# Kernel tuning notes

Hardware: AMD Instinct MI355X
Metric: run time of the kernel (lower is better)

## Reference

```python
import jax, jax.numpy as jnp
import numpy as np

EPS = 1e-5
NUM_GROUPS = 32
NUM_HEADS = 8

def group_norm(x, w, b):
    # x: (B, C, H, W), 32 groups, affine per-channel
    B, C, H, W = x.shape
    xg = x.reshape(B, NUM_GROUPS, C // NUM_GROUPS, H, W)
    mu = xg.mean(axis=(2, 3, 4), keepdims=True)
    var = xg.var(axis=(2, 3, 4), keepdims=True)
    xn = ((xg - mu) * jax.lax.rsqrt(var + EPS)).reshape(B, C, H, W)
    return xn * w[None, :, None, None] + b[None, :, None, None]

def conv1x1(x, w, b):
    # 1x1 conv == per-pixel linear; w: (out, in), x: (B, C, H, W)
    return jnp.einsum('oc,bchw->bohw', w, x) + b[None, :, None, None]

def setup_inputs() -> dict:
    key = jax.random.key(0)
    ks = jax.random.split(key, 4)
    B, C, H, W = 2, 512, 64, 64
    s = 1.0 / np.sqrt(C)
    return {
        'x': jax.random.normal(ks[0], (B, C, H, W), jnp.float32),
        'gn_w': jnp.ones((C,), jnp.float32),
        'gn_b': jnp.zeros((C,), jnp.float32),
        'wq': jax.random.normal(ks[1], (C, C), jnp.float32) * s,
        'bq': jnp.zeros((C,), jnp.float32),
        'wkv': jax.random.normal(ks[2], (2 * C, C), jnp.float32) * s,
        'bkv': jnp.zeros((2 * C,), jnp.float32),
        'wo': jax.random.normal(ks[3], (C, C), jnp.float32) * s,
        'bo': jnp.zeros((C,), jnp.float32),
    }

def reference(x, gn_w, gn_b, wq, bq, wkv, bkv, wo, bo):
    B, C, H, W = x.shape
    hd = C // NUM_HEADS  # head_dim
    residual = x
    x_norm = group_norm(x, gn_w, gn_b)
    q = conv1x1(x_norm, wq, bq).reshape(B, NUM_HEADS, hd, H * W)
    kv = conv1x1(x_norm, wkv, bkv)
    k, v = jnp.split(kv, 2, axis=1)
    k = k.reshape(B, NUM_HEADS, hd, H * W)
    v = v.reshape(B, NUM_HEADS, hd, H * W)
    scale = hd ** (-0.5)
    attn = jnp.einsum('bhdi,bhdj->bhij', q, k) * scale
    attn = jax.nn.softmax(attn, axis=-1)
    out = jnp.einsum('bhij,bhdj->bhdi', attn, v).reshape(B, C, H, W)
    out = conv1x1(out, wo, bo)
    return out + residual
```

## Files before the change

### kernel.cpp

```cpp
#include <hip/hip_runtime.h>
#include <cmath>

typedef __bf16 bf16x8 __attribute__((ext_vector_type(8)));
typedef __bf16 bf16x4 __attribute__((ext_vector_type(4)));
typedef float  f32x4  __attribute__((ext_vector_type(4)));

static __device__ __forceinline__ f32x4 mfma16(bf16x8 a, bf16x8 b, f32x4 c) {
    return __builtin_amdgcn_mfma_f32_16x16x32_bf16(a, b, c, 0, 0, 0);
}

static __device__ __forceinline__ float fast_exp2(float x) {
#if __has_builtin(__builtin_amdgcn_exp2f)
    return __builtin_amdgcn_exp2f(x);
#else
    return exp2f(x);
#endif
}

#define OFF_STATS 0
#define OFF_W     4096
#define OFF_XNT   (OFF_W + 2u*1024*1024)
#define OFF_QKT   (OFF_XNT + 8u*1024*1024)
#define OFF_V     (OFF_QKT + 16u*1024*1024)
#define OFF_OP    (OFF_V + 8u*1024*1024)
#define CHUNK_O   4194304u
#define CHUNK_L   65536u

__global__ __launch_bounds__(256) void cvt_w(const float* __restrict__ wq,
                                             const float* __restrict__ wkv,
                                             const float* __restrict__ wo,
                                             __bf16* __restrict__ dst) {
    int i = blockIdx.x * 256 + threadIdx.x;
    if (i < 262144)      dst[i] = (__bf16)wq[i];
    else if (i < 786432) dst[i] = (__bf16)wkv[i - 262144];
    else                 dst[i] = (__bf16)wo[i - 786432];
}

__global__ __launch_bounds__(256) void gn_stats(const float* __restrict__ x,
                                                float* __restrict__ stats) {
    int blk = blockIdx.x;
    int bg = blk >> 2, chunk = blk & 3;
    const float* base = x + (size_t)bg * 65536 + (size_t)chunk * 16384;
    float s = 0.f, ss = 0.f;
    for (int i = threadIdx.x; i < 4096; i += 256) {
        float4 v = ((const float4*)base)[i];
        s  += v.x + v.y + v.z + v.w;
        ss += v.x*v.x + v.y*v.y + v.z*v.z + v.w*v.w;
    }
    #pragma unroll
    for (int off = 1; off < 64; off <<= 1) {
        s  += __shfl_xor(s,  off);
        ss += __shfl_xor(ss, off);
    }
    __shared__ float red[8];
    int wave = threadIdx.x >> 6;
    if ((threadIdx.x & 63) == 0) { red[wave*2] = s; red[wave*2+1] = ss; }
    __syncthreads();
    if (threadIdx.x == 0) {
        float S  = red[0] + red[2] + red[4] + red[6];
        float SS = red[1] + red[3] + red[5] + red[7];
        atomicAdd(&stats[bg*2],     S);
        atomicAdd(&stats[bg*2 + 1], SS);
    }
}

__global__ __launch_bounds__(256) void gn_apply(const float* __restrict__ x,
                                                const float* __restrict__ stats,
                                                const float* __restrict__ w,
                                                const float* __restrict__ bgn,
                                                __bf16* __restrict__ xnT) {
    int p0 = blockIdx.x * 64, c0 = blockIdx.y * 64, b = blockIdx.z;
    int tid = threadIdx.x, lane = tid & 63, wave = tid >> 6;
    __shared__ float t[64][69];
    #pragma unroll
    for (int i = 0; i < 16; ++i) {
        int cc = i * 4 + wave;
        int c  = c0 + cc;
        int g  = (b << 5) + (c >> 4);
        float mu  = stats[g*2] * (1.f/65536.f);
        float var = stats[g*2+1] * (1.f/65536.f) - mu*mu;
        float rstd = rsqrtf(var + 1e-5f);
        float val = x[((size_t)(b*512 + c) << 12) + p0 + lane];
        t[cc][lane] = (val - mu) * rstd * w[c] + bgn[c];
    }
    __syncthreads();
    #pragma unroll
    for (int i = 0; i < 16; ++i) {
        int pp = i * 4 + wave;
        xnT[((size_t)(b*4096 + p0 + pp) << 9) + c0 + lane] = (__bf16)t[lane][pp];
    }
}

__global__ __launch_bounds__(256) void gemm128_kernel(
    const __bf16* __restrict__ A, const __bf16* __restrict__ B,
    const float* __restrict__ bias, const float* __restrict__ bias2, int nsplit,
    float scale0, void* __restrict__ out,
    int N, int K, long long strideA, long long strideO) {
    const int bz = blockIdx.z;
    A += strideA * bz;
    const int m0 = blockIdx.x * 128, n0 = blockIdx.y * 128;
    const int tid = threadIdx.x, lane = tid & 63, wave = tid >> 6;
    const int quad = lane >> 4, l16 = lane & 15;
    const int wm = (wave >> 1) * 64, wn = (wave & 1) * 64;

    __shared__ __attribute__((aligned(16))) __bf16 lds_a[128][40];
    __shared__ __attribute__((aligned(16))) __bf16 lds_b[128][40];

    f32x4 acc[4][4];
    #pragma unroll
    for (int mt = 0; mt < 4; ++mt)
        #pragma unroll
        for (int nt = 0; nt < 4; ++nt)
            #pragma unroll
            for (int r = 0; r < 4; ++r) acc[mt][nt][r] = 0.f;

    const int row_s = tid >> 2;
    const int kc    = (tid & 3) << 3;

    uint4 ra0, ra1, rb0, rb1;
    const __bf16* Abase = A + (size_t)(m0 + row_s) * K + kc;
    const __bf16* Bbase = B + (size_t)(n0 + row_s) * K + kc;
    ra0 = *(const uint4*)Abase;
    ra1 = *(const uint4*)(Abase + (size_t)64 * K);
    rb0 = *(const uint4*)Bbase;
    rb1 = *(const uint4*)(Bbase + (size_t)64 * K);

    for (int kt = 0; kt < K; kt += 32) {
        *(uint4*)&lds_a[row_s][kc]      = ra0;
        *(uint4*)&lds_a[row_s + 64][kc] = ra1;
        *(uint4*)&lds_b[row_s][kc]      = rb0;
        *(uint4*)&lds_b[row_s + 64][kc] = rb1;
        __syncthreads();
        if (kt + 32 < K) {
            ra0 = *(const uint4*)(Abase + kt + 32);
            ra1 = *(const uint4*)(Abase + kt + 32 + (size_t)64 * K);
            rb0 = *(const uint4*)(Bbase + kt + 32);
            rb1 = *(const uint4*)(Bbase + kt + 32 + (size_t)64 * K);
        }
        bf16x8 af[4], bfr[4];
        #pragma unroll
        for (int mt = 0; mt < 4; ++mt)
            af[mt] = *(const bf16x8*)&lds_a[wm + mt*16 + l16][quad*8];
        #pragma unroll
        for (int nt = 0; nt < 4; ++nt)
            bfr[nt] = *(const bf16x8*)&lds_b[wn + nt*16 + l16][quad*8];
        #pragma unroll
        for (int mt = 0; mt < 4; ++mt)
            #pragma unroll
            for (int nt = 0; nt < 4; ++nt)
                acc[mt][nt] = mfma16(af[mt], bfr[nt], acc[mt][nt]);
        __syncthreads();
    }

    #pragma unroll
    for (int mt = 0; mt < 4; ++mt) {
        const int mrow = m0 + wm + mt*16 + quad*4;
        #pragma unroll
        for (int nt = 0; nt < 4; ++nt) {
            const int ncol = n0 + wn + nt*16 + l16;
            #pragma unroll
            for (int r = 0; r < 4; ++r) {
                const int m = mrow + r;
                float bval = (ncol < nsplit) ? bias[ncol] : bias2[ncol - nsplit];
                float val = acc[mt][nt][r] + bval;
                if (ncol < nsplit) val *= scale0;
                ((__bf16*)out)[(size_t)strideO * bz + (size_t)m * N + ncol] = (__bf16)val;
            }
        }
    }
}

template<int OUT_F32, int HAS_RES>
__global__ __launch_bounds__(256) void gemm64_kernel(
    const __bf16* __restrict__ A, const __bf16* __restrict__ B,
    const float* __restrict__ bias, const float* __restrict__ res,
    void* __restrict__ out,
    int N, int K, long long strideB, long long strideO) {
    const int bz = blockIdx.z;
    B += strideB * bz;
    const int m0 = blockIdx.x * 64, n0 = blockIdx.y * 128;
    const int tid = threadIdx.x, lane = tid & 63, wave = tid >> 6;
    const int quad = lane >> 4, l16 = lane & 15;
    const int wn = wave * 32;

    __shared__ __attribute__((aligned(16))) __bf16 lds_a[64][40];
    __shared__ __attribute__((aligned(16))) __bf16 lds_b[128][40];

    f32x4 acc[4][2];
    #pragma unroll
    for (int mt = 0; mt < 4; ++mt)
        #pragma unroll
        for (int nt = 0; nt < 2; ++nt)
            #pragma unroll
            for (int r = 0; r < 4; ++r) acc[mt][nt][r] = 0.f;

    const int row_s = tid >> 2;
    const int kc    = (tid & 3) << 3;

    uint4 ra0, rb0, rb1;
    const __bf16* Abase = A + (size_t)(m0 + row_s) * K + kc;
    const __bf16* Bbase = B + (size_t)(n0 + row_s) * K + kc;
    ra0 = *(const uint4*)Abase;
    rb0 = *(const uint4*)Bbase;
    rb1 = *(const uint4*)(Bbase + (size_t)64 * K);

    for (int kt = 0; kt < K; kt += 32) {
        *(uint4*)&lds_a[row_s][kc]      = ra0;
        *(uint4*)&lds_b[row_s][kc]      = rb0;
        *(uint4*)&lds_b[row_s + 64][kc] = rb1;
        __syncthreads();
        if (kt + 32 < K) {
            ra0 = *(const uint4*)(Abase + kt + 32);
            rb0 = *(const uint4*)(Bbase + kt + 32);
            rb1 = *(const uint4*)(Bbase + kt + 32 + (size_t)64 * K);
        }
        bf16x8 af[4], bfr[2];
        #pragma unroll
        for (int mt = 0; mt < 4; ++mt)
            af[mt] = *(const bf16x8*)&lds_a[mt*16 + l16][quad*8];
        #pragma unroll
        for (int nt = 0; nt < 2; ++nt)
            bfr[nt] = *(const bf16x8*)&lds_b[wn + nt*16 + l16][quad*8];
        #pragma unroll
        for (int mt = 0; mt < 4; ++mt)
            #pragma unroll
            for (int nt = 0; nt < 2; ++nt)
                acc[mt][nt] = mfma16(af[mt], bfr[nt], acc[mt][nt]);
        __syncthreads();
    }

    #pragma unroll
    for (int mt = 0; mt < 4; ++mt) {
        const int mrow = m0 + mt*16 + quad*4;
        #pragma unroll
        for (int nt = 0; nt < 2; ++nt) {
            const int ncol = n0 + wn + nt*16 + l16;
            #pragma unroll
            for (int r = 0; r < 4; ++r) {
                const int m = mrow + r;
                float val = acc[mt][nt][r] + bias[m];
                const size_t idx = (size_t)strideO * bz + (size_t)m * N + ncol;
                if constexpr (HAS_RES) val += res[idx];
                if constexpr (OUT_F32) ((float*)out)[idx] = val;
                else ((__bf16*)out)[idx] = (__bf16)val;
            }
        }
    }
}

template<int NCH>
__global__ __launch_bounds__(256, 3) void attn_kernel(const __bf16* __restrict__ qkT,
                                                      const __bf16* __restrict__ v,
                                                      __bf16* __restrict__ attnT,
                                                      __bf16* __restrict__ Opart,
                                                      float* __restrict__ Lpart) {
    const int b = blockIdx.y >> 3, h = blockIdx.y & 7;
    const int chunk = (NCH > 1) ? blockIdx.z : 0;
    const int NITER = 64 / NCH;
    const int kt0 = chunk * (4096 / NCH);
    const int tid = threadIdx.x;
    const int wave = tid >> 6, lane = tid & 63;
    const int quad = lane >> 4, l16 = lane & 15;
    const int qbase = blockIdx.x * 256 + wave * 64;

    const __bf16* qkTb = qkT + ((size_t)b << 22);
    const __bf16* vb   = v   + ((size_t)b << 21);

    __shared__ __attribute__((aligned(16))) __bf16 lds_k[64][64];
    __shared__ __attribute__((aligned(16))) __bf16 lds_v[80][64];
    __shared__ __attribute__((aligned(16))) __bf16 lds_p[4][64][68];

    bf16x8 aq[4][2];
    #pragma unroll
    for (int mt = 0; mt < 4; ++mt) {
        const __bf16* qrow = qkTb + (size_t)(qbase + mt*16 + l16) * 1024 + h*64 + quad*8;
        aq[mt][0] = *(const bf16x8*)qrow;
        aq[mt][1] = *(const bf16x8*)(qrow + 32);
    }
    f32x4 o[4][5];
    #pragma unroll
    for (int mt = 0; mt < 4; ++mt)
        #pragma unroll
        for (int dt = 0; dt < 5; ++dt)
            #pragma unroll
            for (int r = 0; r < 4; ++r) o[mt][dt][r] = 0.f;
    const f32x4 kZero = {0.f, 0.f, 0.f, 0.f};

    const int srow = tid >> 2;
    const int sc   = tid & 3;
    const int sw0  = ( sc      ^ (srow & 7)) * 8;
    const int sw1  = ((sc + 4) ^ (srow & 7)) * 8;

    const __bf16* kg0 = qkTb + (size_t)srow * 1024 + 512 + h*64 + sc*8;
    const __bf16* vg0 = vb + ((size_t)(h*64 + srow) << 12) + sc*8;

    if (tid < 64) lds_v[64][tid] = (__bf16)1.0f;

    uint4 ck0, ck1, cv0, cv1;
    {
        const __bf16* kg = kg0 + (size_t)kt0 * 1024;
        const __bf16* vg = vg0 + kt0;
        ck0 = *(const uint4*)kg; ck1 = *(const uint4*)(kg + 32);
        cv0 = *(const uint4*)vg; cv1 = *(const uint4*)(vg + 32);
    }

    for (int it = 0; it < NITER; ++it) {
        *(uint4*)&lds_k[srow][sw0] = ck0;
        *(uint4*)&lds_k[srow][sw1] = ck1;
        *(uint4*)&lds_v[srow][sw0] = cv0;
        *(uint4*)&lds_v[srow][sw1] = cv1;
        __syncthreads();
        if (it + 1 < NITER) {
            const int kt = kt0 + (it + 1) * 64;
            const __bf16* kg = kg0 + (size_t)kt * 1024;
            const __bf16* vg = vg0 + kt;
            ck0 = *(const uint4*)kg; ck1 = *(const uint4*)(kg + 32);
            cv0 = *(const uint4*)vg; cv1 = *(const uint4*)(vg + 32);
        }

        #pragma unroll
        for (int nt = 0; nt < 4; ++nt) {
            const int kr = nt*16 + l16;
            bf16x8 bk0 = *(const bf16x8*)&lds_k[kr][( quad      ^ (l16 & 7)) * 8];
            bf16x8 bk1 = *(const bf16x8*)&lds_k[kr][((4 + quad) ^ (l16 & 7)) * 8];
            #pragma unroll
            for (int mt = 0; mt < 4; ++mt) {
                f32x4 s = mfma16(bk1, aq[mt][1], mfma16(bk0, aq[mt][0], kZero));
                f32x4 p;
                #pragma unroll
                for (int r = 0; r < 4; ++r) p[r] = fast_exp2(s[r]);
                bf16x4 pb = __builtin_convertvector(p, bf16x4);
                *(bf16x4*)&lds_p[wave][mt*16 + l16][nt*16 + quad*4] = pb;
            }
        }

        #pragma unroll
        for (int kc = 0; kc < 2; ++kc) {
            bf16x8 pa[4];
            #pragma unroll
            for (int mt = 0; mt < 4; ++mt) {
                bf16x4 plo = *(const bf16x4*)&lds_p[wave][mt*16 + l16][kc*32 + quad*8];
                bf16x4 phi = *(const bf16x4*)&lds_p[wave][mt*16 + l16][kc*32 + quad*8 + 4];
                pa[mt] = __builtin_shufflevector(plo, phi, 0, 1, 2, 3, 4, 5, 6, 7);
            }
            #pragma unroll
            for (int dt = 0; dt < 5; ++dt) {
                bf16x8 bv = *(const bf16x8*)&lds_v[dt*16 + l16][((kc*4 + quad) ^ (l16 & 7)) * 8];
                #pragma unroll
                for (int mt = 0; mt < 4; ++mt)
                    o[mt][dt] = mfma16(pa[mt], bv, o[mt][dt]);
            }
        }
        __syncthreads();
    }

    if constexpr (NCH > 1) {
        __bf16* Ob = Opart + (size_t)chunk * CHUNK_O;
        #pragma unroll
        for (int mt = 0; mt < 4; ++mt)
            #pragma unroll
            for (int dt = 0; dt < 4; ++dt)
                #pragma unroll
                for (int r = 0; r < 4; ++r) {
                    size_t row = (size_t)b * 4096 + qbase + mt*16 + quad*4 + r;
                    Ob[(row << 9) + (h << 6) + dt*16 + l16] = (__bf16)o[mt][dt][r];
                }
        if (l16 == 0) {
            #pragma unroll
            for (int mt = 0; mt < 4; ++mt)
                #pragma unroll
                for (int r = 0; r < 4; ++r) {
                    int p = qbase + mt*16 + quad*4 + r;
                    Lpart[(size_t)chunk * CHUNK_L + (size_t)(((b*8 + h)) << 12) + p] = o[mt][4][r];
                }
        }
    } else {
        #pragma unroll
        for (int mt = 0; mt < 4; ++mt) {
            float inv[4];
            #pragma unroll
            for (int r = 0; r < 4; ++r)
                inv[r] = 1.f / __shfl(o[mt][4][r], lane & 48);
            #pragma unroll
            for (int dt = 0; dt < 4; ++dt)
                #pragma unroll
                for (int r = 0; r < 4; ++r) {
                    size_t row = (size_t)b * 4096 + qbase + mt*16 + quad*4 + r;
                    attnT[(row << 9) + (h << 6) + dt*16 + l16] = (__bf16)(o[mt][dt][r] * inv[r]);
                }
        }
    }
}

template<int NCH>
__global__ __launch_bounds__(256) void attn_combine(const __bf16* __restrict__ Opart,
                                                    const float* __restrict__ Lpart,
                                                    __bf16* __restrict__ attnT) {
    int i = blockIdx.x * 256 + threadIdx.x;
    int c4 = i & 127;
    int p  = (i >> 7) & 4095;
    int b  = i >> 19;
    int h  = c4 >> 4;
    size_t lidx = (size_t)((b*8 + h) << 12) + p;
    float l = 0.f;
    #pragma unroll
    for (int ch = 0; ch < NCH; ++ch) l += Lpart[(size_t)ch * CHUNK_L + lidx];
    float inv = 1.f / l;
    size_t oi = ((size_t)(b*4096 + p) << 9) + c4*4;
    float acc[4] = {0.f, 0.f, 0.f, 0.f};
    #pragma unroll
    for (int ch = 0; ch < NCH; ++ch) {
        bf16x4 ov = *(const bf16x4*)&Opart[(size_t)ch * CHUNK_O + oi];
        #pragma unroll
        for (int r = 0; r < 4; ++r) acc[r] += (float)ov[r];
    }
    bf16x4 rv;
    #pragma unroll
    for (int r = 0; r < 4; ++r) rv[r] = (__bf16)(acc[r] * inv);
    *(bf16x4*)&attnT[oi] = rv;
}

extern "C" void kernel_launch(void* const* d_in, const int* in_sizes, int n_in,
                              void* d_out, int out_size, void* d_ws, size_t ws_size,
                              hipStream_t stream) {
    const float* x   = (const float*)d_in[0];
    const float* gnw = (const float*)d_in[1];
    const float* gnb = (const float*)d_in[2];
    const float* wq  = (const float*)d_in[3];
    const float* bq  = (const float*)d_in[4];
    const float* wkv = (const float*)d_in[5];
    const float* bkv = (const float*)d_in[6];
    const float* wo  = (const float*)d_in[7];
    const float* bo  = (const float*)d_in[8];
    float* out = (float*)d_out;

    char* ws = (char*)d_ws;
    float*  stats  = (float*)(ws + OFF_STATS);
    __bf16* wbf    = (__bf16*)(ws + OFF_W);
    __bf16* wkv_bf = wbf + 262144;
    __bf16* wo_bf  = wbf + 786432;
    __bf16* xnT    = (__bf16*)(ws + OFF_XNT);
    __bf16* qkT    = (__bf16*)(ws + OFF_QKT);
    __bf16* vv     = (__bf16*)(ws + OFF_V);
    __bf16* Opart  = (__bf16*)(ws + OFF_OP);
    __bf16* attnT  = xnT;

    const size_t need4 = (size_t)OFF_OP + 4u * (CHUNK_O * 2 + CHUNK_L * 4);
    const size_t need2 = (size_t)OFF_OP + 2u * (CHUNK_O * 2 + CHUNK_L * 4);
    const int nch = (ws_size >= need4) ? 4 : (ws_size >= need2 ? 2 : 1);
    float* Lpart = (float*)(ws + OFF_OP + (size_t)nch * CHUNK_O * 2);

    hipMemsetAsync(stats, 0, 512, stream);
    cvt_w<<<4096, 256, 0, stream>>>(wq, wkv, wo, wbf);
    gn_stats<<<256, 256, 0, stream>>>(x, stats);
    gn_apply<<<dim3(64, 8, 2), 256, 0, stream>>>(x, stats, gnw, gnb, xnT);

    const long long S = 2097152LL;
    const long long S2 = 4194304LL;
    gemm128_kernel<<<dim3(32, 8, 2), 256, 0, stream>>>(
        xnT, wbf, bq, bkv, 512, 0.125f * 1.44269504f, qkT, 1024, 512, S, S2);
    gemm64_kernel<0,0><<<dim3(8, 32, 2), 256, 0, stream>>>(
        wkv_bf + 262144, xnT, bkv + 512, nullptr, vv, 4096, 512, S, S);

    if (nch == 4) {
        attn_kernel<4><<<dim3(16, 16, 4), 256, 0, stream>>>(qkT, vv, nullptr, Opart, Lpart);
        attn_combine<4><<<4096, 256, 0, stream>>>(Opart, Lpart, attnT);
    } else if (nch == 2) {
        attn_kernel<2><<<dim3(16, 16, 2), 256, 0, stream>>>(qkT, vv, nullptr, Opart, Lpart);
        attn_combine<2><<<4096, 256, 0, stream>>>(Opart, Lpart, attnT);
    } else {
        attn_kernel<1><<<dim3(16, 16, 1), 256, 0, stream>>>(qkT, vv, attnT, nullptr, nullptr);
    }

    gemm64_kernel<1,1><<<dim3(8, 32, 2), 256, 0, stream>>>(
        wo_bf, attnT, bo, x, out, 4096, 512, S, S);
}
```

Measured before the change: 229.3 us.

## Fuse fp32 weight conversion into GEMM loaders and shrink attention P buffer

```diff
diff --git a/kernel.cpp b/kernel.cpp
--- a/kernel.cpp
+++ b/kernel.cpp
@@ -17,24 +17,20 @@
 #endif
 }
 
+static __device__ __forceinline__ bf16x8 cvt8(float4 a, float4 b) {
+    bf16x8 r;
+    r[0] = (__bf16)a.x; r[1] = (__bf16)a.y; r[2] = (__bf16)a.z; r[3] = (__bf16)a.w;
+    r[4] = (__bf16)b.x; r[5] = (__bf16)b.y; r[6] = (__bf16)b.z; r[7] = (__bf16)b.w;
+    return r;
+}
+
 #define OFF_STATS 0
-#define OFF_W     4096
-#define OFF_XNT   (OFF_W + 2u*1024*1024)
+#define OFF_XNT   (4096 + 2u*1024*1024)
 #define OFF_QKT   (OFF_XNT + 8u*1024*1024)
 #define OFF_V     (OFF_QKT + 16u*1024*1024)
 #define OFF_OP    (OFF_V + 8u*1024*1024)
 #define CHUNK_O   4194304u
 #define CHUNK_L   65536u
-
-__global__ __launch_bounds__(256) void cvt_w(const float* __restrict__ wq,
-                                             const float* __restrict__ wkv,
-                                             const float* __restrict__ wo,
-                                             __bf16* __restrict__ dst) {
-    int i = blockIdx.x * 256 + threadIdx.x;
-    if (i < 262144)      dst[i] = (__bf16)wq[i];
-    else if (i < 786432) dst[i] = (__bf16)wkv[i - 262144];
-    else                 dst[i] = (__bf16)wo[i - 786432];
-}
 
 __global__ __launch_bounds__(256) void gn_stats(const float* __restrict__ x,
                                                 float* __restrict__ stats) {
@@ -91,17 +87,18 @@
     }
 }
 
-__global__ __launch_bounds__(256) void gemm128_kernel(
-    const __bf16* __restrict__ A, const __bf16* __restrict__ B,
-    const float* __restrict__ bias, const float* __restrict__ bias2, int nsplit,
-    float scale0, void* __restrict__ out,
-    int N, int K, long long strideA, long long strideO) {
+__global__ __launch_bounds__(256) void gemm_qk_kernel(
+    const __bf16* __restrict__ A, const float* __restrict__ Wq,
+    const float* __restrict__ Wk,
+    const float* __restrict__ bq, const float* __restrict__ bk,
+    float qscale, __bf16* __restrict__ out) {
     const int bz = blockIdx.z;
-    A += strideA * bz;
+    A += (size_t)bz * 2097152;
     const int m0 = blockIdx.x * 128, n0 = blockIdx.y * 128;
     const int tid = threadIdx.x, lane = tid & 63, wave = tid >> 6;
     const int quad = lane >> 4, l16 = lane & 15;
     const int wm = (wave >> 1) * 64, wn = (wave & 1) * 64;
+    const int K = 512;
 
     __shared__ __attribute__((aligned(16))) __bf16 lds_a[128][40];
     __shared__ __attribute__((aligned(16))) __bf16 lds_b[128][40];
@@ -117,25 +114,29 @@
     const int row_s = tid >> 2;
     const int kc    = (tid & 3) << 3;
 
-    uint4 ra0, ra1, rb0, rb1;
     const __bf16* Abase = A + (size_t)(m0 + row_s) * K + kc;
-    const __bf16* Bbase = B + (size_t)(n0 + row_s) * K + kc;
+    const int br0 = n0 + row_s, br1 = br0 + 64;
+    const float* B0 = (br0 < 512) ? (Wq + (size_t)br0 * K + kc) : (Wk + (size_t)(br0 - 512) * K + kc);
+    const float* B1 = (br1 < 512) ? (Wq + (size_t)br1 * K + kc) : (Wk + (size_t)(br1 - 512) * K + kc);
+
+    uint4 ra0, ra1;
+    float4 f0a, f0b, f1a, f1b;
     ra0 = *(const uint4*)Abase;
     ra1 = *(const uint4*)(Abase + (size_t)64 * K);
-    rb0 = *(const uint4*)Bbase;
-    rb1 = *(const uint4*)(Bbase + (size_t)64 * K);
+    f0a = *(const float4*)B0;      f0b = *(const float4*)(B0 + 4);
+    f1a = *(const float4*)B1;      f1b = *(const float4*)(B1 + 4);
 
     for (int kt = 0; kt < K; kt += 32) {
-        *(uint4*)&lds_a[row_s][kc]      = ra0;
-        *(uint4*)&lds_a[row_s + 64][kc] = ra1;
-        *(uint4*)&lds_b[row_s][kc]      = rb0;
-        *(uint4*)&lds_b[row_s + 64][kc] = rb1;
+        *(uint4*)&lds_a[row_s][kc]       = ra0;
+        *(uint4*)&lds_a[row_s + 64][kc]  = ra1;
+        *(bf16x8*)&lds_b[row_s][kc]      = cvt8(f0a, f0b);
+        *(bf16x8*)&lds_b[row_s + 64][kc] = cvt8(f1a, f1b);
         __syncthreads();
         if (kt + 32 < K) {
             ra0 = *(const uint4*)(Abase + kt + 32);
             ra1 = *(const uint4*)(Abase + kt + 32 + (size_t)64 * K);
-            rb0 = *(const uint4*)(Bbase + kt + 32);
-            rb1 = *(const uint4*)(Bbase + kt + 32 + (size_t)64 * K);
+            f0a = *(const float4*)(B0 + kt + 32); f0b = *(const float4*)(B0 + kt + 36);
+            f1a = *(const float4*)(B1 + kt + 32); f1b = *(const float4*)(B1 + kt + 36);
         }
         bf16x8 af[4], bfr[4];
         #pragma unroll
@@ -161,10 +162,10 @@
             #pragma unroll
             for (int r = 0; r < 4; ++r) {
                 const int m = mrow + r;
-                float bval = (ncol < nsplit) ? bias[ncol] : bias2[ncol - nsplit];
+                float bval = (ncol < 512) ? bq[ncol] : bk[ncol - 512];
                 float val = acc[mt][nt][r] + bval;
-                if (ncol < nsplit) val *= scale0;
-                ((__bf16*)out)[(size_t)strideO * bz + (size_t)m * N + ncol] = (__bf16)val;
+                if (ncol < 512) val *= qscale;
+                out[(size_t)bz * 4194304 + (size_t)m * 1024 + ncol] = (__bf16)val;
             }
         }
     }
@@ -172,7 +173,7 @@
 
 template<int OUT_F32, int HAS_RES>
 __global__ __launch_bounds__(256) void gemm64_kernel(
-    const __bf16* __restrict__ A, const __bf16* __restrict__ B,
+    const float* __restrict__ A, const __bf16* __restrict__ B,
     const float* __restrict__ bias, const float* __restrict__ res,
     void* __restrict__ out,
     int N, int K, long long strideB, long long strideO) {
@@ -197,20 +198,21 @@
     const int row_s = tid >> 2;
     const int kc    = (tid & 3) << 3;
 
-    uint4 ra0, rb0, rb1;
-    const __bf16* Abase = A + (size_t)(m0 + row_s) * K + kc;
+    const float*  Abase = A + (size_t)(m0 + row_s) * K + kc;
     const __bf16* Bbase = B + (size_t)(n0 + row_s) * K + kc;
-    ra0 = *(const uint4*)Abase;
+    float4 fa, fb;
+    uint4 rb0, rb1;
+    fa  = *(const float4*)Abase;  fb = *(const float4*)(Abase + 4);
     rb0 = *(const uint4*)Bbase;
     rb1 = *(const uint4*)(Bbase + (size_t)64 * K);
 
     for (int kt = 0; kt < K; kt += 32) {
-        *(uint4*)&lds_a[row_s][kc]      = ra0;
+        *(bf16x8*)&lds_a[row_s][kc]     = cvt8(fa, fb);
         *(uint4*)&lds_b[row_s][kc]      = rb0;
         *(uint4*)&lds_b[row_s + 64][kc] = rb1;
         __syncthreads();
         if (kt + 32 < K) {
-            ra0 = *(const uint4*)(Abase + kt + 32);
+            fa  = *(const float4*)(Abase + kt + 32); fb = *(const float4*)(Abase + kt + 36);
             rb0 = *(const uint4*)(Bbase + kt + 32);
             rb1 = *(const uint4*)(Bbase + kt + 32 + (size_t)64 * K);
         }
@@ -249,7 +251,7 @@
 }
 
 template<int NCH>
-__global__ __launch_bounds__(256, 3) void attn_kernel(const __bf16* __restrict__ qkT,
+__global__ __launch_bounds__(256, 4) void attn_kernel(const __bf16* __restrict__ qkT,
                                                       const __bf16* __restrict__ v,
                                                       __bf16* __restrict__ attnT,
                                                       __bf16* __restrict__ Opart,
@@ -268,7 +270,7 @@
 
     __shared__ __attribute__((aligned(16))) __bf16 lds_k[64][64];
     __shared__ __attribute__((aligned(16))) __bf16 lds_v[80][64];
-    __shared__ __attribute__((aligned(16))) __bf16 lds_p[4][64][68];
+    __shared__ __attribute__((aligned(16))) __bf16 lds_p[4][64][36];
 
     bf16x8 aq[4][2];
     #pragma unroll
@@ -319,28 +321,28 @@
         }
 
         #pragma unroll
-        for (int nt = 0; nt < 4; ++nt) {
-            const int kr = nt*16 + l16;
-            bf16x8 bk0 = *(const bf16x8*)&lds_k[kr][( quad      ^ (l16 & 7)) * 8];
-            bf16x8 bk1 = *(const bf16x8*)&lds_k[kr][((4 + quad) ^ (l16 & 7)) * 8];
+        for (int kc = 0; kc < 2; ++kc) {
+            #pragma unroll
+            for (int ntl = 0; ntl < 2; ++ntl) {
+                const int nt = kc*2 + ntl;
+                const int kr = nt*16 + l16;
+                bf16x8 bk0 = *(const bf16x8*)&lds_k[kr][( quad      ^ (l16 & 7)) * 8];
+                bf16x8 bk1 = *(const bf16x8*)&lds_k[kr][((4 + quad) ^ (l16 & 7)) * 8];
+                #pragma unroll
+                for (int mt = 0; mt < 4; ++mt) {
+                    f32x4 s = mfma16(bk1, aq[mt][1], mfma16(bk0, aq[mt][0], kZero));
+                    f32x4 p;
+                    #pragma unroll
+                    for (int r = 0; r < 4; ++r) p[r] = fast_exp2(s[r]);
+                    bf16x4 pb = __builtin_convertvector(p, bf16x4);
+                    *(bf16x4*)&lds_p[wave][mt*16 + l16][ntl*16 + quad*4] = pb;
+                }
+            }
+            bf16x8 pa[4];
             #pragma unroll
             for (int mt = 0; mt < 4; ++mt) {
-                f32x4 s = mfma16(bk1, aq[mt][1], mfma16(bk0, aq[mt][0], kZero));
-                f32x4 p;
-                #pragma unroll
-                for (int r = 0; r < 4; ++r) p[r] = fast_exp2(s[r]);
-                bf16x4 pb = __builtin_convertvector(p, bf16x4);
-                *(bf16x4*)&lds_p[wave][mt*16 + l16][nt*16 + quad*4] = pb;
-            }
-        }
-
-        #pragma unroll
-        for (int kc = 0; kc < 2; ++kc) {
-            bf16x8 pa[4];
-            #pragma unroll
-            for (int mt = 0; mt < 4; ++mt) {
-                bf16x4 plo = *(const bf16x4*)&lds_p[wave][mt*16 + l16][kc*32 + quad*8];
-                bf16x4 phi = *(const bf16x4*)&lds_p[wave][mt*16 + l16][kc*32 + quad*8 + 4];
+                bf16x4 plo = *(const bf16x4*)&lds_p[wave][mt*16 + l16][quad*8];
+                bf16x4 phi = *(const bf16x4*)&lds_p[wave][mt*16 + l16][quad*8 + 4];
                 pa[mt] = __builtin_shufflevector(plo, phi, 0, 1, 2, 3, 4, 5, 6, 7);
             }
             #pragma unroll
@@ -371,7 +373,7 @@
                 #pragma unroll
                 for (int r = 0; r < 4; ++r) {
                     int p = qbase + mt*16 + quad*4 + r;
-                    Lpart[(size_t)chunk * CHUNK_L + (size_t)(((b*8 + h)) << 12) + p] = o[mt][4][r];
+                    Lpart[(size_t)chunk * CHUNK_L + (size_t)((b*8 + h) << 12) + p] = o[mt][4][r];
                 }
         }
     } else {
@@ -436,9 +438,6 @@
 
     char* ws = (char*)d_ws;
     float*  stats  = (float*)(ws + OFF_STATS);
-    __bf16* wbf    = (__bf16*)(ws + OFF_W);
-    __bf16* wkv_bf = wbf + 262144;
-    __bf16* wo_bf  = wbf + 786432;
     __bf16* xnT    = (__bf16*)(ws + OFF_XNT);
     __bf16* qkT    = (__bf16*)(ws + OFF_QKT);
     __bf16* vv     = (__bf16*)(ws + OFF_V);
@@ -451,16 +450,14 @@
     float* Lpart = (float*)(ws + OFF_OP + (size_t)nch * CHUNK_O * 2);
 
     hipMemsetAsync(stats, 0, 512, stream);
-    cvt_w<<<4096, 256, 0, stream>>>(wq, wkv, wo, wbf);
     gn_stats<<<256, 256, 0, stream>>>(x, stats);
     gn_apply<<<dim3(64, 8, 2), 256, 0, stream>>>(x, stats, gnw, gnb, xnT);
 
     const long long S = 2097152LL;
-    const long long S2 = 4194304LL;
-    gemm128_kernel<<<dim3(32, 8, 2), 256, 0, stream>>>(
-        xnT, wbf, bq, bkv, 512, 0.125f * 1.44269504f, qkT, 1024, 512, S, S2);
+    gemm_qk_kernel<<<dim3(32, 8, 2), 256, 0, stream>>>(
+        xnT, wq, wkv, bq, bkv, 0.125f * 1.44269504f, qkT);
     gemm64_kernel<0,0><<<dim3(8, 32, 2), 256, 0, stream>>>(
-        wkv_bf + 262144, xnT, bkv + 512, nullptr, vv, 4096, 512, S, S);
+        wkv + 262144, xnT, bkv + 512, nullptr, vv, 4096, 512, S, S);
 
     if (nch == 4) {
         attn_kernel<4><<<dim3(16, 16, 4), 256, 0, stream>>>(qkT, vv, nullptr, Opart, Lpart);
@@ -473,5 +470,5 @@
     }
 
     gemm64_kernel<1,1><<<dim3(8, 32, 2), 256, 0, stream>>>(
-        wo_bf, attnT, bo, x, out, 4096, 512, S, S);
-}
+        wo, attnT, bo, x, out, 4096, 512, S, S);
+}
```

New measurement: 487.5 us. +112.6%, slower.
